# Kernel tuning notes

Measured on AMD Instinct MI355X. Metric: run time of the kernel, lower is better.

The kernel has to match this reference:

```python
import jax, jax.numpy as jnp
import numpy as np

B, C, S, H, W = 1, 256, 64, 32, 128
BLOCKS, HEADS, DH = 2, 8, 32
SCALE = DH ** (-0.5)


def layer_norm(x, w, b, eps=1e-5):
    mu = jnp.mean(x, axis=-1, keepdims=True)
    var = jnp.var(x, axis=-1, keepdims=True)
    return (x - mu) * jax.lax.rsqrt(var + eps) * w + b


def generate_y_for_attn(y, u):
    # y: (B,C,H,W), u: (B,S,S) float -> (B, S^2, 2H, C)
    Bv, Cv, Hv, Wv = y.shape
    Sv = u.shape[1]
    uf = jnp.floor(u).reshape(Bv, Sv * Sv)
    u_left = jnp.clip(uf, 0, Wv - 1).astype(jnp.int32)
    u_right = jnp.clip(uf + 1, 0, Wv - 1).astype(jnp.int32)
    yf = y.reshape(Bv, Cv * Hv, Wv)

    def gather_w(idx):
        idxb = jnp.broadcast_to(idx[:, None, :], (Bv, Cv * Hv, Sv * Sv))
        return jnp.take_along_axis(yf, idxb, axis=2).reshape(Bv, Cv, Hv, Sv * Sv)

    ys = jnp.concatenate([gather_w(u_left), gather_w(u_right)], axis=2)  # (B,C,2H,S2)
    return ys.transpose(0, 3, 2, 1)  # (B, S2, 2H, C)


def cross_attention(x, y, p, i):
    # x: (B,M,C), y: (B,M,N,C)
    q = layer_norm(x, p['ln_q_w'][i], p['ln_q_b'][i]) @ p['Wq'][i]        # (B,M,HD)
    k = layer_norm(y, p['ln_k_w'][i], p['ln_k_b'][i]) @ p['Wk'][i]        # (B,M,N,HD)
    v = layer_norm(y, p['ln_v_w'][i], p['ln_v_b'][i]) @ p['Wv'][i]        # (B,M,N,HD)
    Bv, M, _ = q.shape
    N = k.shape[2]
    q = q.reshape(Bv, M, HEADS, DH)
    k = k.reshape(Bv, M, N, HEADS, DH)
    v = v.reshape(Bv, M, N, HEADS, DH)
    dot = SCALE * jnp.einsum('bmhd,bmnhd->bhmn', q, k)                    # (B,H,M,N)
    attn = jax.nn.softmax(dot, axis=-1)
    a = jnp.einsum('bhmn,bmnhd->bmhd', attn, v).reshape(Bv, M, HEADS * DH)
    z = a @ p['Wproj'][i] + p['bproj'][i]
    z = layer_norm(z, p['ln_pre_w'][i], p['ln_pre_b'][i])
    h = jax.nn.gelu(z @ p['Wm1'][i] + p['bm1'][i], approximate=False)
    z = z + (h @ p['Wm2'][i] + p['bm2'][i])
    return layer_norm(z, p['ln_post_w'][i], p['ln_post_b'][i])


def setup_inputs() -> dict:
    key = jax.random.key(0)
    ks = jax.random.split(key, 16)
    std = 0.02
    inp = {
        'grd2sat': jax.random.normal(ks[0], (B, C, S, S), jnp.float32),
        'grd_x': jax.random.normal(ks[1], (B, C, H, W), jnp.float32),
        'u': jax.random.uniform(ks[2], (B, S, S), jnp.float32) * (W - 1),
        'ln_q_w': jnp.ones((BLOCKS, C)), 'ln_q_b': jnp.zeros((BLOCKS, C)),
        'ln_k_w': jnp.ones((BLOCKS, C)), 'ln_k_b': jnp.zeros((BLOCKS, C)),
        'ln_v_w': jnp.ones((BLOCKS, C)), 'ln_v_b': jnp.zeros((BLOCKS, C)),
        'Wq': std * jax.random.normal(ks[3], (BLOCKS, C, HEADS * DH)),
        'Wk': std * jax.random.normal(ks[4], (BLOCKS, C, HEADS * DH)),
        'Wv': std * jax.random.normal(ks[5], (BLOCKS, C, HEADS * DH)),
        'Wproj': std * jax.random.normal(ks[6], (BLOCKS, HEADS * DH, C)),
        'bproj': jnp.zeros((BLOCKS, C)),
        'ln_pre_w': jnp.ones((BLOCKS, C)), 'ln_pre_b': jnp.zeros((BLOCKS, C)),
        'Wm1': std * jax.random.normal(ks[7], (BLOCKS, C, 2 * C)),
        'bm1': jnp.zeros((BLOCKS, 2 * C)),
        'Wm2': std * jax.random.normal(ks[8], (BLOCKS, 2 * C, C)),
        'bm2': jnp.zeros((BLOCKS, C)),
        'ln_post_w': jnp.ones((BLOCKS, C)), 'ln_post_b': jnp.zeros((BLOCKS, C)),
    }
    return inp


def reference(grd2sat, grd_x, u, ln_q_w, ln_q_b, ln_k_w, ln_k_b, ln_v_w, ln_v_b,
              Wq, Wk, Wv, Wproj, bproj, ln_pre_w, ln_pre_b, Wm1, bm1, Wm2, bm2,
              ln_post_w, ln_post_b):
    p = dict(ln_q_w=ln_q_w, ln_q_b=ln_q_b, ln_k_w=ln_k_w, ln_k_b=ln_k_b,
             ln_v_w=ln_v_w, ln_v_b=ln_v_b, Wq=Wq, Wk=Wk, Wv=Wv, Wproj=Wproj,
             bproj=bproj, ln_pre_w=ln_pre_w, ln_pre_b=ln_pre_b, Wm1=Wm1, bm1=bm1,
             Wm2=Wm2, bm2=bm2, ln_post_w=ln_post_w, ln_post_b=ln_post_b)
    y_attn = generate_y_for_attn(grd_x, u)               # (B, S^2, 2H, C)
    x = grd2sat.reshape(B, C, S * S).transpose(0, 2, 1)  # (B, M, C)
    for i in range(BLOCKS):
        # (Swin self-attention layer omitted; cross-attention stack only.)
        x = cross_attention(x, y_attn, p, i)
    out = x.transpose(0, 2, 1).reshape(B, C, S, S)
    # L2 normalize over channel dim
    norm = jnp.sqrt(jnp.sum(out * out, axis=1, keepdims=True))
    return out / jnp.maximum(norm, 1e-12)
```

## Files before the change

### kernel.cpp

```cpp
#include <hip/hip_runtime.h>
#include <math.h>


#define C_DIM 256
#define M_DIM 4096
#define W_DIM 128
#define H_DIM 32
#define ATT_SCALE 0.17677669529663687f

typedef __attribute__((ext_vector_type(8))) short short8;
typedef __attribute__((ext_vector_type(4))) short short4v;
typedef __attribute__((ext_vector_type(4))) float floatx4;

__device__ __forceinline__ unsigned short f2bf(float f) {
    unsigned u = __float_as_uint(f);
    unsigned r = (u + 0x7fffu + ((u >> 16) & 1u)) >> 16;
    return (unsigned short)r;
}
__device__ __forceinline__ float gelu_exact(float x) {
    return 0.5f * x * (1.0f + erff(x * 0.70710678118654752f));
}

struct PrepArgs {
    const float* grd2sat; float* xcur;
    const float* grd_x;   float* yhat;
    const float* u; int* perm; int4* chunks; int* nchunks;
    const float* win[12]; unsigned short* wout[12]; const float* wlnw[12];
    int wR[12], wC[12], wbase[13];
    const float* fW[10]; const float* flnb[10]; const float* fbase[10];
    float* fout[10];
    int fN[10], fwcol[10], focol[10];
};

__global__ __launch_bounds__(256) void prep_kernel(PrepArgs a) {
    __shared__ float smemf[9024];
    int b = blockIdx.x, t = threadIdx.x;
    if (b < 256) {
        float (*tile)[65] = (float(*)[65])smemf;
        int m0 = (b & 63) << 6, c0 = (b >> 6) << 6;
        for (int it = 0; it < 16; ++it) {
            int idx = it * 256 + t;
            int co = idx >> 6, mo = idx & 63;
            tile[co][mo] = a.grd2sat[(size_t)(c0 + co) * M_DIM + m0 + mo];
        }
        __syncthreads();
        for (int it = 0; it < 16; ++it) {
            int idx = it * 256 + t;
            int mo = idx >> 6, co = idx & 63;
            a.xcur[(size_t)(m0 + mo) * C_DIM + c0 + co] = tile[co][mo];
        }
    } else if (b < 384) {
        int idx = b - 256;
        int h = idx & 31, w0 = (idx >> 5) << 5;
        float (*tile)[33] = (float(*)[33])smemf;
        float (*ps)[32] = (float(*)[32])(smemf + 8448);
        float (*pss)[32] = (float(*)[32])(smemf + 8704);
        float* mu_s = smemf + 8960;
        float* rs_s = smemf + 8992;
        int wo = t & 31, cb = t >> 5;
        for (int it = 0; it < 32; ++it) {
            int c = it * 8 + cb;
            tile[c][wo] = a.grd_x[(size_t)c * (H_DIM * W_DIM) + h * W_DIM + w0 + wo];
        }
        __syncthreads();
        {
            int w = t & 31, part = t >> 5;
            float s = 0.f, ss = 0.f;
            for (int c = part * 32; c < part * 32 + 32; ++c) {
                float x = tile[c][w];
                s += x; ss += x * x;
            }
            ps[part][w] = s; pss[part][w] = ss;
        }
        __syncthreads();
        if (t < 32) {
            float s = 0.f, ss = 0.f;
            for (int p = 0; p < 8; ++p) { s += ps[p][t]; ss += pss[p][t]; }
            float mu = s * (1.f / 256.f);
            float var = ss * (1.f / 256.f) - mu * mu;
            mu_s[t] = mu;
            rs_s[t] = rsqrtf(var + 1e-5f);
        }
        __syncthreads();
        for (int jj = 0; jj < 32; ++jj) {
            float mu = mu_s[jj], rs = rs_s[jj];
            a.yhat[((size_t)(w0 + jj) * H_DIM + h) * C_DIM + t] =
                (tile[t][jj] - mu) * rs;
        }
    } else if (b < 1408) {
        int wI = b - 384;
        int e = 0;
        while (wI >= a.wbase[e + 1]) ++e;
        int tl = wI - a.wbase[e];
        int tilesC = a.wC[e] >> 5;
        int tr = tl / tilesC, tc = tl - tr * tilesC;
        int r0 = tr << 5, c0 = tc << 5;
        const float* in = a.win[e];
        unsigned short* out = a.wout[e];
        const float* lnw = a.wlnw[e];
        int R = a.wR[e], Cc = a.wC[e];
        float (*tile)[33] = (float(*)[33])smemf;
        int rl = t >> 3, cq = (t & 7) << 2;
        float4 v = *(const float4*)&in[(size_t)(r0 + rl) * Cc + c0 + cq];
        if (lnw) {
            float s = lnw[r0 + rl];
            v.x *= s; v.y *= s; v.z *= s; v.w *= s;
        }
        tile[rl][cq + 0] = v.x;
        tile[rl][cq + 1] = v.y;
        tile[rl][cq + 2] = v.z;
        tile[rl][cq + 3] = v.w;
        __syncthreads();
        int cl = t >> 3, rq = (t & 7) << 2;
        ushort4 o;
        o.x = f2bf(tile[rq + 0][cl]);
        o.y = f2bf(tile[rq + 1][cl]);
        o.z = f2bf(tile[rq + 2][cl]);
        o.w = f2bf(tile[rq + 3][cl]);
        *(ushort4*)&out[(size_t)(c0 + cl) * R + r0 + rq] = o;
    } else if (b < 1418) {
        int jj = b - 1408;
        int N = a.fN[jj];
        int wcol = a.fwcol[jj] + t;
        const float* W = a.fW[jj];
        const float* lb = a.flnb[jj];
        float s = a.fbase[jj] ? a.fbase[jj][wcol] : 0.f;
        for (int k = 0; k < 256; ++k) s += lb[k] * W[(size_t)k * N + wcol];
        a.fout[jj][a.focol[jj] + t] = s;
    } else {
        int* hist = (int*)smemf;
        int* cur = (int*)smemf + 128;
        unsigned short* wlb = (unsigned short*)((int*)smemf + 256);
        if (t < 128) hist[t] = 0;
        __syncthreads();
        for (int it = 0; it < 16; ++it) {
            int m = it * 256 + t;
            int wl = (int)floorf(a.u[m]);
            wl = max(0, min(wl, 126));
            wlb[m] = (unsigned short)wl;
            atomicAdd(&hist[wl], 1);
        }
        __syncthreads();
        if (t == 0) {
            int run = 0, nc = 0;
            for (int bkt = 0; bkt < 127; ++bkt) {
                int c = hist[bkt];
                cur[bkt] = run;
                int q0 = run;
                while (c > 0) {
                    int take = min(c, 32);
                    a.chunks[nc] = make_int4(bkt, q0, take, 0);
                    ++nc; q0 += take; c -= take;
                }
                run += hist[bkt];
            }
            *a.nchunks = nc;
        }
        __syncthreads();
        for (int it = 0; it < 16; ++it) {
            int m = it * 256 + t;
            int wl = wlb[m];
            int pos = atomicAdd(&cur[wl], 1);
            a.perm[pos] = m;
        }
    }
}

struct GJ {
    const void* A; const unsigned short* Bt;
    const float* bias; const float* aw; const float* ab;
    const float* rw; const float* rb; const float* res;
    float* wrz; void* out; unsigned short* out2;
    int K, N;
};

template <int LN, int EPI, int OUTM, bool WRZ, bool ABF16>
__device__ __forceinline__ void gemm_core(const GJ& j, short (*As)[264],
                                          short (*Bs)[264], int bm, int by) {
    int t = threadIdx.x;
    int bn = by << 6;
    int wv = t >> 6, lane = t & 63;
    int mt = wv & 1, nt0 = (wv >> 1) << 1;
    int quad = lane >> 4, l16 = lane & 15;
    floatx4 acc0 = {0.f, 0.f, 0.f, 0.f};
    floatx4 acc1 = {0.f, 0.f, 0.f, 0.f};
    const int K = j.K;
    for (int kc = 0; kc < K; kc += 256) {
        if (kc) __syncthreads();
        if (ABF16) {
            int ar = t >> 3, cq = (t & 7) << 5;
            const unsigned short* ap =
                (const unsigned short*)j.A + (size_t)(bm + ar) * K + kc + cq;
#pragma unroll
            for (int c = 0; c < 4; ++c)
                *(uint4*)&As[ar][cq + (c << 3)] = *(const uint4*)(ap + (c << 3));
        } else {
            int ar = t >> 3, cq = (t & 7) << 2;
            const float* ap = (const float*)j.A + (size_t)(bm + ar) * K + kc + cq;
            float4 v[8];
#pragma unroll
            for (int g = 0; g < 8; ++g) v[g] = *(const float4*)(ap + g * 32);
            if (LN >= 1) {
                float s = 0.f, ss = 0.f;
#pragma unroll
                for (int g = 0; g < 8; ++g) {
                    s += v[g].x + v[g].y + v[g].z + v[g].w;
                    ss += v[g].x * v[g].x + v[g].y * v[g].y + v[g].z * v[g].z +
                          v[g].w * v[g].w;
                }
#pragma unroll
                for (int o = 1; o < 8; o <<= 1) {
                    s += __shfl_xor(s, o, 64);
                    ss += __shfl_xor(ss, o, 64);
                }
                float mu = s * (1.f / 256.f);
                float rs = rsqrtf(ss * (1.f / 256.f) - mu * mu + 1e-5f);
#pragma unroll
                for (int g = 0; g < 8; ++g) {
                    v[g].x = (v[g].x - mu) * rs;
                    v[g].y = (v[g].y - mu) * rs;
                    v[g].z = (v[g].z - mu) * rs;
                    v[g].w = (v[g].w - mu) * rs;
                }
                if (LN == 2) {
                    float s2 = 0.f, ss2 = 0.f;
#pragma unroll
                    for (int g = 0; g < 8; ++g) {
                        float4 w4 = *(const float4*)(j.aw + cq + g * 32);
                        float4 b4 = *(const float4*)(j.ab + cq + g * 32);
                        v[g].x = v[g].x * w4.x + b4.x;
                        v[g].y = v[g].y * w4.y + b4.y;
                        v[g].z = v[g].z * w4.z + b4.z;
                        v[g].w = v[g].w * w4.w + b4.w;
                        s2 += v[g].x + v[g].y + v[g].z + v[g].w;
                        ss2 += v[g].x * v[g].x + v[g].y * v[g].y +
                               v[g].z * v[g].z + v[g].w * v[g].w;
                    }
#pragma unroll
                    for (int o = 1; o < 8; o <<= 1) {
                        s2 += __shfl_xor(s2, o, 64);
                        ss2 += __shfl_xor(ss2, o, 64);
                    }
                    float mu2 = s2 * (1.f / 256.f);
                    float rs2 = rsqrtf(ss2 * (1.f / 256.f) - mu2 * mu2 + 1e-5f);
#pragma unroll
                    for (int g = 0; g < 8; ++g) {
                        v[g].x = (v[g].x - mu2) * rs2;
                        v[g].y = (v[g].y - mu2) * rs2;
                        v[g].z = (v[g].z - mu2) * rs2;
                        v[g].w = (v[g].w - mu2) * rs2;
                    }
                }
            }
            if (WRZ) {
                if (by == 0) {
#pragma unroll
                    for (int g = 0; g < 8; ++g)
                        *(float4*)&j.wrz[(size_t)(bm + ar) * 256 + cq + g * 32] =
                            v[g];
                }
            }
#pragma unroll
            for (int g = 0; g < 8; ++g) {
                short4v o;
                o[0] = (short)f2bf(v[g].x);
                o[1] = (short)f2bf(v[g].y);
                o[2] = (short)f2bf(v[g].z);
                o[3] = (short)f2bf(v[g].w);
                *(short4v*)&As[ar][cq + g * 32] = o;
            }
        }
        {
            int br = t >> 2, cq2 = (t & 3) << 3;
            const unsigned short* bp = j.Bt + (size_t)(bn + br) * K + kc + cq2;
#pragma unroll
            for (int g = 0; g < 8; ++g)
                *(short8*)&Bs[br][cq2 + g * 32] = *(const short8*)(bp + g * 32);
        }
        __syncthreads();
#pragma unroll
        for (int k0 = 0; k0 < 8; ++k0) {
            short8 aa = *(const short8*)&As[(mt << 4) + l16][(k0 << 5) + (quad << 3)];
            short8 b0 = *(const short8*)&Bs[(nt0 << 4) + l16][(k0 << 5) + (quad << 3)];
            short8 b1 =
                *(const short8*)&Bs[((nt0 + 1) << 4) + l16][(k0 << 5) + (quad << 3)];
            acc0 = __builtin_amdgcn_mfma_f32_16x16x32_bf16(aa, b0, acc0, 0, 0, 0);
            acc1 = __builtin_amdgcn_mfma_f32_16x16x32_bf16(aa, b1, acc1, 0, 0, 0);
        }
    }
#pragma unroll
    for (int jj = 0; jj < 2; ++jj) {
        const floatx4 accv = jj ? acc1 : acc0;
        int col = bn + ((nt0 + jj) << 4) + l16;
        float bv = j.bias ? j.bias[col] : 0.f;
#pragma unroll
        for (int r = 0; r < 4; ++r) {
            int row = bm + (mt << 4) + (quad << 2) + r;
            float v = accv[r] + bv;
            if (EPI == 1) v = gelu_exact(v);
            if (EPI == 2)
                v += j.res[(size_t)row * 256 + col] * j.rw[col] + j.rb[col];
            if (OUTM == 0) {
                ((float*)j.out)[(size_t)row * j.N + col] = v;
            } else if (OUTM == 1) {
                ((unsigned short*)j.out)[(size_t)row * j.N + col] = f2bf(v);
            } else {
                if (col < 256)
                    ((unsigned short*)j.out)[(size_t)row * 256 + col] = f2bf(v);
                else
                    j.out2[(size_t)(col - 256) * M_DIM + row] = f2bf(v);
            }
        }
    }
}

template <int MODE>
__global__ __launch_bounds__(256) void gemm_mode(GJ j0, GJ j1, GJ j2) {
    __shared__ short As[32][264];
    __shared__ short Bs[64][264];
    int bm = blockIdx.x << 5;
    if (MODE == 0) {
        if ((int)blockIdx.y < 4)
            gemm_core<1, 0, 1, false, false>(j0, As, Bs, bm, blockIdx.y);
        else if ((int)blockIdx.y < 12)
            gemm_core<0, 0, 2, false, false>(j1, As, Bs, bm, blockIdx.y - 4);
        else
            gemm_core<0, 0, 2, false, false>(j2, As, Bs, bm, blockIdx.y - 12);
    } else if (MODE == 1) {
        gemm_core<2, 0, 1, false, false>(j0, As, Bs, bm, blockIdx.y);
    } else if (MODE == 2) {
        gemm_core<0, 0, 0, false, true>(j0, As, Bs, bm, blockIdx.y);
    } else if (MODE == 3) {
        gemm_core<1, 1, 1, true, false>(j0, As, Bs, bm, blockIdx.y);
    } else {
        gemm_core<0, 2, 0, false, true>(j0, As, Bs, bm, blockIdx.y);
    }
}

__global__ __launch_bounds__(256) void attn_kernel(
    const unsigned short* __restrict__ Qb, const unsigned short* __restrict__ Kt,
    const unsigned short* __restrict__ Vt, const int* __restrict__ perm,
    const int4* __restrict__ chunks, const int* __restrict__ nchunks,
    unsigned short* __restrict__ Ao) {
    __shared__ float S[32][69];
    __shared__ short Pb[32][72];
    __shared__ int gperm[32];
    if ((int)blockIdx.x >= *nchunks) return;
    int4 cd = chunks[blockIdx.x];
    int wl = cd.x, qstart = cd.y, qcnt = cd.z;
    int t = threadIdx.x;
    if (t < 32) gperm[t] = (t < qcnt) ? perm[qstart + t] : perm[qstart];
    __syncthreads();
    int wv = t >> 6, lane = t & 63, quad = lane >> 4, l16 = lane & 15;
    int mt = wv & 1, nt0 = (wv >> 1) << 1;
    int ntP = wv >> 1;
    const unsigned short* qp = Qb + (size_t)gperm[(mt << 4) + l16] * 256;
    const unsigned short* kp0 =
        Kt + ((size_t)((wl << 5) + (nt0 << 4) + l16)) * 256;
    const unsigned short* kp1 = kp0 + (16 * 256);
    int sq = t >> 3, sg = t & 7;
    int hb = (int)blockIdx.y << 2;
#pragma unroll 1
    for (int h = hb; h < hb + 4; ++h) {
        {
            short8 aa = *(const short8*)(qp + (h << 5) + (quad << 3));
            short8 b0 = *(const short8*)(kp0 + (h << 5) + (quad << 3));
            short8 b1 = *(const short8*)(kp1 + (h << 5) + (quad << 3));
            floatx4 z = {0.f, 0.f, 0.f, 0.f};
            floatx4 c0 = __builtin_amdgcn_mfma_f32_16x16x32_bf16(aa, b0, z, 0, 0, 0);
            floatx4 c1 = __builtin_amdgcn_mfma_f32_16x16x32_bf16(aa, b1, z, 0, 0, 0);
#pragma unroll
            for (int r = 0; r < 4; ++r) {
                int row = (mt << 4) + (quad << 2) + r;
                S[row][(nt0 << 4) + l16] = c0[r];
                S[row][((nt0 + 1) << 4) + l16] = c1[r];
            }
        }
        __syncthreads();
        {
            float e[8];
            float s = 0.f;
#pragma unroll
            for (int c = 0; c < 8; ++c) {
                e[c] = __expf(S[sq][(sg << 3) + c] * ATT_SCALE);
                s += e[c];
            }
            s += __shfl_xor(s, 1, 64);
            s += __shfl_xor(s, 2, 64);
            s += __shfl_xor(s, 4, 64);
            float ri = 1.f / s;
#pragma unroll
            for (int c = 0; c < 8; ++c)
                Pb[sq][(sg << 3) + c] = (short)f2bf(e[c] * ri);
        }
        __syncthreads();
        {
            const unsigned short* vp =
                Vt + ((size_t)((h << 5) + (ntP << 4) + l16)) * M_DIM + (wl << 5);
            floatx4 acc = {0.f, 0.f, 0.f, 0.f};
#pragma unroll
            for (int ks = 0; ks < 2; ++ks) {
                short8 pa =
                    *(const short8*)&Pb[(mt << 4) + l16][(ks << 5) + (quad << 3)];
                short8 vb = *(const short8*)(vp + (ks << 5) + (quad << 3));
                acc = __builtin_amdgcn_mfma_f32_16x16x32_bf16(pa, vb, acc, 0, 0, 0);
            }
#pragma unroll
            for (int r = 0; r < 4; ++r) {
                int q = (mt << 4) + (quad << 2) + r;
                if (q < qcnt)
                    Ao[(size_t)gperm[q] * 256 + (h << 5) + (ntP << 4) + l16] =
                        f2bf(acc[r]);
            }
        }
    }
}

__global__ __launch_bounds__(256) void out_kernel(const float* __restrict__ X,
                                                  const float* __restrict__ w,
                                                  const float* __restrict__ b,
                                                  float* __restrict__ out) {
    __shared__ float tile[64][65];
    int t = threadIdx.x;
    int mo = t >> 2, q = t & 3;
    int m0 = blockIdx.x << 6;
    const float* p = X + (size_t)(m0 + mo) * C_DIM + (q << 6);
    float4 v[16];
    float s = 0.f, ss = 0.f;
#pragma unroll
    for (int c = 0; c < 16; ++c) {
        v[c] = *(const float4*)(p + c * 4);
        s += v[c].x + v[c].y + v[c].z + v[c].w;
        ss += v[c].x * v[c].x + v[c].y * v[c].y + v[c].z * v[c].z + v[c].w * v[c].w;
    }
    s += __shfl_xor(s, 1, 64); s += __shfl_xor(s, 2, 64);
    ss += __shfl_xor(ss, 1, 64); ss += __shfl_xor(ss, 2, 64);
    float mu = s * (1.f / 256.f);
    float rs = rsqrtf(ss * (1.f / 256.f) - mu * mu + 1e-5f);
    float ss2 = 0.f;
#pragma unroll
    for (int c = 0; c < 16; ++c) {
        float4 w4 = *(const float4*)&w[(q << 6) + c * 4];
        float4 b4 = *(const float4*)&b[(q << 6) + c * 4];
        v[c].x = (v[c].x - mu) * rs * w4.x + b4.x;
        v[c].y = (v[c].y - mu) * rs * w4.y + b4.y;
        v[c].z = (v[c].z - mu) * rs * w4.z + b4.z;
        v[c].w = (v[c].w - mu) * rs * w4.w + b4.w;
        ss2 += v[c].x * v[c].x + v[c].y * v[c].y + v[c].z * v[c].z + v[c].w * v[c].w;
    }
    ss2 += __shfl_xor(ss2, 1, 64); ss2 += __shfl_xor(ss2, 2, 64);
    float sc = 1.f / fmaxf(sqrtf(ss2), 1e-12f);
    for (int cc = 0; cc < 4; ++cc) {
        if (q == cc) {
#pragma unroll
            for (int c = 0; c < 16; ++c) {
                tile[mo][c * 4 + 0] = v[c].x * sc;
                tile[mo][c * 4 + 1] = v[c].y * sc;
                tile[mo][c * 4 + 2] = v[c].z * sc;
                tile[mo][c * 4 + 3] = v[c].w * sc;
            }
        }
        __syncthreads();
        for (int it = 0; it < 16; ++it) {
            int idx = it * 256 + t;
            int co = idx >> 6, mr = idx & 63;
            out[(size_t)((cc << 6) + co) * M_DIM + m0 + mr] = tile[mr][co];
        }
        __syncthreads();
    }
}

extern "C" void kernel_launch(void* const* d_in, const int* in_sizes, int n_in,
                              void* d_out, int out_size, void* d_ws, size_t ws_size,
                              hipStream_t stream) {
    const float* grd2sat = (const float*)d_in[0];
    const float* grd_x   = (const float*)d_in[1];
    const float* u       = (const float*)d_in[2];
    const float* ln_q_w  = (const float*)d_in[3];
    const float* ln_q_b  = (const float*)d_in[4];
    const float* ln_k_w  = (const float*)d_in[5];
    const float* ln_k_b  = (const float*)d_in[6];
    const float* ln_v_w  = (const float*)d_in[7];
    const float* ln_v_b  = (const float*)d_in[8];
    const float* Wq      = (const float*)d_in[9];
    const float* Wk      = (const float*)d_in[10];
    const float* Wv      = (const float*)d_in[11];
    const float* Wproj   = (const float*)d_in[12];
    const float* bproj   = (const float*)d_in[13];
    const float* ln_pre_w = (const float*)d_in[14];
    const float* ln_pre_b = (const float*)d_in[15];
    const float* Wm1     = (const float*)d_in[16];
    const float* bm1     = (const float*)d_in[17];
    const float* Wm2     = (const float*)d_in[18];
    const float* bm2     = (const float*)d_in[19];
    const float* ln_post_w = (const float*)d_in[20];
    const float* ln_post_b = (const float*)d_in[21];

    float* ws   = (float*)d_ws;
    float* yhat = ws;
    float* xcur = ws + 1048576;
    float* zq   = ws + 2097152;
    float* zbuf = ws + 3145728;
    unsigned short* hbuf = (unsigned short*)(ws + 4194304);
    unsigned short* Qb   = (unsigned short*)(ws + 5242880);
    unsigned short* abuf = (unsigned short*)(ws + 5767168);
    unsigned short* Ktab0 = (unsigned short*)(ws + 6291456);
    unsigned short* Vt0   = (unsigned short*)(ws + 6815744);
    unsigned short* Ktab1 = (unsigned short*)(ws + 7340032);
    unsigned short* Vt1   = (unsigned short*)(ws + 7864320);
    unsigned short* Bt    = (unsigned short*)(ws + 8388608);
    float* biasbuf = ws + 8912896;
    int*  perm    = (int*)(ws + 8915456);
    int4* chunks  = (int4*)(ws + 8919552);
    int*  nchunks = (int*)(ws + 8921600);
    const size_t BS = 524288;
    const size_t OQ = 0, OKV = 65536, OP = 196608, OM1 = 262144, OM2 = 393216;

    dim3 b256(256);

    PrepArgs pa;
    pa.grd2sat = grd2sat; pa.xcur = xcur;
    pa.grd_x = grd_x;     pa.yhat = yhat;
    pa.u = u; pa.perm = perm; pa.chunks = chunks; pa.nchunks = nchunks;
    {
        int base = 0;
        for (int i = 0; i < 2; ++i) {
            int e = 6 * i;
            unsigned short* bt = Bt + i * BS;
            pa.win[e+0] = Wq + i * 65536;    pa.wout[e+0] = bt + OQ;
            pa.wlnw[e+0] = ln_q_w + i * 256; pa.wR[e+0] = 256; pa.wC[e+0] = 256;
            pa.win[e+1] = Wk + i * 65536;    pa.wout[e+1] = bt + OKV;
            pa.wlnw[e+1] = ln_k_w + i * 256; pa.wR[e+1] = 256; pa.wC[e+1] = 256;
            pa.win[e+2] = Wv + i * 65536;    pa.wout[e+2] = bt + OKV + 65536;
            pa.wlnw[e+2] = ln_v_w + i * 256; pa.wR[e+2] = 256; pa.wC[e+2] = 256;
            pa.win[e+3] = Wproj + i * 65536; pa.wout[e+3] = bt + OP;
            pa.wlnw[e+3] = nullptr;          pa.wR[e+3] = 256; pa.wC[e+3] = 256;
            pa.win[e+4] = Wm1 + i * 131072;  pa.wout[e+4] = bt + OM1;
            pa.wlnw[e+4] = ln_pre_w + i * 256; pa.wR[e+4] = 256; pa.wC[e+4] = 512;
            pa.win[e+5] = Wm2 + i * 131072;  pa.wout[e+5] = bt + OM2;
            pa.wlnw[e+5] = nullptr;          pa.wR[e+5] = 512; pa.wC[e+5] = 256;
        }
        for (int e = 0; e < 12; ++e) {
            pa.wbase[e] = base;
            base += (pa.wR[e] >> 5) * (pa.wC[e] >> 5);
        }
        pa.wbase[12] = base;
        for (int i = 0; i < 2; ++i) {
            int jb = 5 * i;
            float* bb = biasbuf + i * 1280;
            pa.fW[jb+0] = Wq + i * 65536; pa.flnb[jb+0] = ln_q_b + i * 256;
            pa.fbase[jb+0] = nullptr; pa.fout[jb+0] = bb;
            pa.fN[jb+0] = 256; pa.fwcol[jb+0] = 0; pa.focol[jb+0] = 0;
            pa.fW[jb+1] = Wk + i * 65536; pa.flnb[jb+1] = ln_k_b + i * 256;
            pa.fbase[jb+1] = nullptr; pa.fout[jb+1] = bb + 256;
            pa.fN[jb+1] = 256; pa.fwcol[jb+1] = 0; pa.focol[jb+1] = 0;
            pa.fW[jb+2] = Wv + i * 65536; pa.flnb[jb+2] = ln_v_b + i * 256;
            pa.fbase[jb+2] = nullptr; pa.fout[jb+2] = bb + 256;
            pa.fN[jb+2] = 256; pa.fwcol[jb+2] = 0; pa.focol[jb+2] = 256;
            pa.fW[jb+3] = Wm1 + i * 131072; pa.flnb[jb+3] = ln_pre_b + i * 256;
            pa.fbase[jb+3] = bm1 + i * 512; pa.fout[jb+3] = bb + 768;
            pa.fN[jb+3] = 512; pa.fwcol[jb+3] = 0; pa.focol[jb+3] = 0;
            pa.fW[jb+4] = Wm1 + i * 131072; pa.flnb[jb+4] = ln_pre_b + i * 256;
            pa.fbase[jb+4] = bm1 + i * 512; pa.fout[jb+4] = bb + 768;
            pa.fN[jb+4] = 512; pa.fwcol[jb+4] = 256; pa.focol[jb+4] = 256;
        }
    }
    prep_kernel<<<1419, b256, 0, stream>>>(pa);

    GJ jz = {};
    for (int i = 0; i < 2; ++i) {
        const unsigned short* bt = Bt + i * BS;
        float* bb = biasbuf + i * 1280;
        unsigned short* Kt = i ? Ktab1 : Ktab0;
        unsigned short* Vt = i ? Vt1 : Vt0;

        GJ jq = {};
        jq.A = xcur; jq.Bt = bt + OQ; jq.bias = bb;
        if (i == 1) { jq.aw = ln_post_w; jq.ab = ln_post_b; }
        jq.out = Qb; jq.K = 256; jq.N = 256;
        if (i == 0) {
            GJ jkv0 = {};
            jkv0.A = yhat; jkv0.Bt = Bt + OKV; jkv0.bias = biasbuf + 256;
            jkv0.out = Ktab0; jkv0.out2 = Vt0; jkv0.K = 256; jkv0.N = 512;
            GJ jkv1 = {};
            jkv1.A = yhat; jkv1.Bt = Bt + BS + OKV; jkv1.bias = biasbuf + 1280 + 256;
            jkv1.out = Ktab1; jkv1.out2 = Vt1; jkv1.K = 256; jkv1.N = 512;
            gemm_mode<0><<<dim3(128, 20), b256, 0, stream>>>(jq, jkv0, jkv1);
        } else {
            gemm_mode<1><<<dim3(128, 4), b256, 0, stream>>>(jq, jz, jz);
        }

        attn_kernel<<<dim3(384, 2), b256, 0, stream>>>(Qb, Kt, Vt, perm, chunks,
                                                       nchunks, abuf);

        GJ jp = {};
        jp.A = abuf; jp.Bt = bt + OP; jp.bias = bproj + i * 256;
        jp.out = zq; jp.K = 256; jp.N = 256;
        gemm_mode<2><<<dim3(128, 4), b256, 0, stream>>>(jp, jz, jz);

        GJ jm1 = {};
        jm1.A = zq; jm1.Bt = bt + OM1; jm1.bias = bb + 768;
        jm1.out = hbuf; jm1.wrz = zbuf; jm1.K = 256; jm1.N = 512;
        gemm_mode<3><<<dim3(128, 8), b256, 0, stream>>>(jm1, jz, jz);

        GJ jm2 = {};
        jm2.A = hbuf; jm2.Bt = bt + OM2; jm2.bias = bm2 + i * 256;
        jm2.res = zbuf; jm2.rw = ln_pre_w + i * 256; jm2.rb = ln_pre_b + i * 256;
        jm2.out = xcur; jm2.K = 512; jm2.N = 256;
        gemm_mode<4><<<dim3(128, 4), b256, 0, stream>>>(jm2, jz, jz);
    }
    out_kernel<<<64, b256, 0, stream>>>(xcur, ln_post_w + 256, ln_post_b + 256,
                                        (float*)d_out);
}
```

Measured before the change: 216.4 us.

## Drop LDS staging in GEMM, load MFMA fragments from global; store yhat as bf16

The GEMM core no longer stages A and B tiles through shared memory. Each wave loads its A fragments straight into registers (with LayerNorm applied in registers) and streams B fragments directly from global memory into the MFMAs. This removes the LDS traffic and barriers at the cost of redundant global reads across waves and higher register pressure. The normalized yhat buffer is now stored as bf16, so the K/V GEMMs read half the bytes via the bf16 A path, and the workspace layout is rearranged to match. A small unroll pragma is also added to the bias-folding loop.

```diff
diff --git a/kernel.cpp b/kernel.cpp
--- a/kernel.cpp
+++ b/kernel.cpp
@@ -23,7 +23,7 @@
 
 struct PrepArgs {
     const float* grd2sat; float* xcur;
-    const float* grd_x;   float* yhat;
+    const float* grd_x;   unsigned short* yhat;
     const float* u; int* perm; int4* chunks; int* nchunks;
     const float* win[12]; unsigned short* wout[12]; const float* wlnw[12];
     int wR[12], wC[12], wbase[13];
@@ -85,7 +85,7 @@
         for (int jj = 0; jj < 32; ++jj) {
             float mu = mu_s[jj], rs = rs_s[jj];
             a.yhat[((size_t)(w0 + jj) * H_DIM + h) * C_DIM + t] =
-                (tile[t][jj] - mu) * rs;
+                f2bf((tile[t][jj] - mu) * rs);
         }
     } else if (b < 1408) {
         int wI = b - 384;
@@ -125,6 +125,7 @@
         const float* W = a.fW[jj];
         const float* lb = a.flnb[jj];
         float s = a.fbase[jj] ? a.fbase[jj][wcol] : 0.f;
+#pragma unroll 8
         for (int k = 0; k < 256; ++k) s += lb[k] * W[(size_t)k * N + wcol];
         a.fout[jj][a.focol[jj] + t] = s;
     } else {
@@ -174,119 +175,122 @@
     int K, N;
 };
 
-template <int LN, int EPI, int OUTM, bool WRZ, bool ABF16>
-__device__ __forceinline__ void gemm_core(const GJ& j, short (*As)[264],
-                                          short (*Bs)[264], int bm, int by) {
+template <int LN, int EPI, int OUTM, bool WRZ, bool ABF16, int K32>
+__device__ __forceinline__ void gemm_core(const GJ& j, int bm, int by) {
+    const int K = K32 * 32;
     int t = threadIdx.x;
     int bn = by << 6;
     int wv = t >> 6, lane = t & 63;
     int mt = wv & 1, nt0 = (wv >> 1) << 1;
     int quad = lane >> 4, l16 = lane & 15;
+    int arow = bm + (mt << 4) + l16;
+
+    short8 afr[K32];
+    if (ABF16) {
+        const unsigned short* ap =
+            (const unsigned short*)j.A + (size_t)arow * K + (quad << 3);
+#pragma unroll
+        for (int k0 = 0; k0 < K32; ++k0)
+            afr[k0] = *(const short8*)(ap + (k0 << 5));
+    } else {
+        const float* apf = (const float*)j.A + (size_t)arow * 256 + (quad << 3);
+        float4 v[16];
+#pragma unroll
+        for (int k0 = 0; k0 < 8; ++k0) {
+            v[2 * k0] = *(const float4*)(apf + (k0 << 5));
+            v[2 * k0 + 1] = *(const float4*)(apf + (k0 << 5) + 4);
+        }
+        if (LN >= 1) {
+            float s = 0.f, ss = 0.f;
+#pragma unroll
+            for (int g = 0; g < 16; ++g) {
+                s += v[g].x + v[g].y + v[g].z + v[g].w;
+                ss += v[g].x * v[g].x + v[g].y * v[g].y + v[g].z * v[g].z +
+                      v[g].w * v[g].w;
+            }
+            s += __shfl_xor(s, 16, 64);
+            s += __shfl_xor(s, 32, 64);
+            ss += __shfl_xor(ss, 16, 64);
+            ss += __shfl_xor(ss, 32, 64);
+            float mu = s * (1.f / 256.f);
+            float rs = rsqrtf(ss * (1.f / 256.f) - mu * mu + 1e-5f);
+#pragma unroll
+            for (int g = 0; g < 16; ++g) {
+                v[g].x = (v[g].x - mu) * rs;
+                v[g].y = (v[g].y - mu) * rs;
+                v[g].z = (v[g].z - mu) * rs;
+                v[g].w = (v[g].w - mu) * rs;
+            }
+            if (LN == 2) {
+                float s2 = 0.f, ss2 = 0.f;
+#pragma unroll
+                for (int k0 = 0; k0 < 8; ++k0) {
+                    float4 w0 = *(const float4*)(j.aw + (k0 << 5) + (quad << 3));
+                    float4 w1 = *(const float4*)(j.aw + (k0 << 5) + (quad << 3) + 4);
+                    float4 b0 = *(const float4*)(j.ab + (k0 << 5) + (quad << 3));
+                    float4 b1 = *(const float4*)(j.ab + (k0 << 5) + (quad << 3) + 4);
+                    float4& x0 = v[2 * k0];
+                    float4& x1 = v[2 * k0 + 1];
+                    x0.x = x0.x * w0.x + b0.x; x0.y = x0.y * w0.y + b0.y;
+                    x0.z = x0.z * w0.z + b0.z; x0.w = x0.w * w0.w + b0.w;
+                    x1.x = x1.x * w1.x + b1.x; x1.y = x1.y * w1.y + b1.y;
+                    x1.z = x1.z * w1.z + b1.z; x1.w = x1.w * w1.w + b1.w;
+                    s2 += x0.x + x0.y + x0.z + x0.w + x1.x + x1.y + x1.z + x1.w;
+                    ss2 += x0.x * x0.x + x0.y * x0.y + x0.z * x0.z + x0.w * x0.w +
+                           x1.x * x1.x + x1.y * x1.y + x1.z * x1.z + x1.w * x1.w;
+                }
+                s2 += __shfl_xor(s2, 16, 64);
+                s2 += __shfl_xor(s2, 32, 64);
+                ss2 += __shfl_xor(ss2, 16, 64);
+                ss2 += __shfl_xor(ss2, 32, 64);
+                float mu2 = s2 * (1.f / 256.f);
+                float rs2 = rsqrtf(ss2 * (1.f / 256.f) - mu2 * mu2 + 1e-5f);
+#pragma unroll
+                for (int g = 0; g < 16; ++g) {
+                    v[g].x = (v[g].x - mu2) * rs2;
+                    v[g].y = (v[g].y - mu2) * rs2;
+                    v[g].z = (v[g].z - mu2) * rs2;
+                    v[g].w = (v[g].w - mu2) * rs2;
+                }
+            }
+        }
+        if (WRZ) {
+            if (by == 0 && wv < 2) {
+#pragma unroll
+                for (int k0 = 0; k0 < 8; ++k0) {
+                    *(float4*)&j.wrz[(size_t)arow * 256 + (k0 << 5) + (quad << 3)] =
+                        v[2 * k0];
+                    *(float4*)&j.wrz[(size_t)arow * 256 + (k0 << 5) + (quad << 3) + 4] =
+                        v[2 * k0 + 1];
+                }
+            }
+        }
+#pragma unroll
+        for (int k0 = 0; k0 < 8; ++k0) {
+            short8 f;
+            f[0] = (short)f2bf(v[2 * k0].x);
+            f[1] = (short)f2bf(v[2 * k0].y);
+            f[2] = (short)f2bf(v[2 * k0].z);
+            f[3] = (short)f2bf(v[2 * k0].w);
+            f[4] = (short)f2bf(v[2 * k0 + 1].x);
+            f[5] = (short)f2bf(v[2 * k0 + 1].y);
+            f[6] = (short)f2bf(v[2 * k0 + 1].z);
+            f[7] = (short)f2bf(v[2 * k0 + 1].w);
+            afr[k0] = f;
+        }
+    }
+
     floatx4 acc0 = {0.f, 0.f, 0.f, 0.f};
     floatx4 acc1 = {0.f, 0.f, 0.f, 0.f};
-    const int K = j.K;
-    for (int kc = 0; kc < K; kc += 256) {
-        if (kc) __syncthreads();
-        if (ABF16) {
-            int ar = t >> 3, cq = (t & 7) << 5;
-            const unsigned short* ap =
-                (const unsigned short*)j.A + (size_t)(bm + ar) * K + kc + cq;
-#pragma unroll
-            for (int c = 0; c < 4; ++c)
-                *(uint4*)&As[ar][cq + (c << 3)] = *(const uint4*)(ap + (c << 3));
-        } else {
-            int ar = t >> 3, cq = (t & 7) << 2;
-            const float* ap = (const float*)j.A + (size_t)(bm + ar) * K + kc + cq;
-            float4 v[8];
-#pragma unroll
-            for (int g = 0; g < 8; ++g) v[g] = *(const float4*)(ap + g * 32);
-            if (LN >= 1) {
-                float s = 0.f, ss = 0.f;
-#pragma unroll
-                for (int g = 0; g < 8; ++g) {
-                    s += v[g].x + v[g].y + v[g].z + v[g].w;
-                    ss += v[g].x * v[g].x + v[g].y * v[g].y + v[g].z * v[g].z +
-                          v[g].w * v[g].w;
-                }
-#pragma unroll
-                for (int o = 1; o < 8; o <<= 1) {
-                    s += __shfl_xor(s, o, 64);
-                    ss += __shfl_xor(ss, o, 64);
-                }
-                float mu = s * (1.f / 256.f);
-                float rs = rsqrtf(ss * (1.f / 256.f) - mu * mu + 1e-5f);
-#pragma unroll
-                for (int g = 0; g < 8; ++g) {
-                    v[g].x = (v[g].x - mu) * rs;
-                    v[g].y = (v[g].y - mu) * rs;
-                    v[g].z = (v[g].z - mu) * rs;
-                    v[g].w = (v[g].w - mu) * rs;
-                }
-                if (LN == 2) {
-                    float s2 = 0.f, ss2 = 0.f;
-#pragma unroll
-                    for (int g = 0; g < 8; ++g) {
-                        float4 w4 = *(const float4*)(j.aw + cq + g * 32);
-                        float4 b4 = *(const float4*)(j.ab + cq + g * 32);
-                        v[g].x = v[g].x * w4.x + b4.x;
-                        v[g].y = v[g].y * w4.y + b4.y;
-                        v[g].z = v[g].z * w4.z + b4.z;
-                        v[g].w = v[g].w * w4.w + b4.w;
-                        s2 += v[g].x + v[g].y + v[g].z + v[g].w;
-                        ss2 += v[g].x * v[g].x + v[g].y * v[g].y +
-                               v[g].z * v[g].z + v[g].w * v[g].w;
-                    }
-#pragma unroll
-                    for (int o = 1; o < 8; o <<= 1) {
-                        s2 += __shfl_xor(s2, o, 64);
-                        ss2 += __shfl_xor(ss2, o, 64);
-                    }
-                    float mu2 = s2 * (1.f / 256.f);
-                    float rs2 = rsqrtf(ss2 * (1.f / 256.f) - mu2 * mu2 + 1e-5f);
-#pragma unroll
-                    for (int g = 0; g < 8; ++g) {
-                        v[g].x = (v[g].x - mu2) * rs2;
-                        v[g].y = (v[g].y - mu2) * rs2;
-                        v[g].z = (v[g].z - mu2) * rs2;
-                        v[g].w = (v[g].w - mu2) * rs2;
-                    }
-                }
-            }
-            if (WRZ) {
-                if (by == 0) {
-#pragma unroll
-                    for (int g = 0; g < 8; ++g)
-                        *(float4*)&j.wrz[(size_t)(bm + ar) * 256 + cq + g * 32] =
-                            v[g];
-                }
-            }
-#pragma unroll
-            for (int g = 0; g < 8; ++g) {
-                short4v o;
-                o[0] = (short)f2bf(v[g].x);
-                o[1] = (short)f2bf(v[g].y);
-                o[2] = (short)f2bf(v[g].z);
-                o[3] = (short)f2bf(v[g].w);
-                *(short4v*)&As[ar][cq + g * 32] = o;
-            }
-        }
-        {
-            int br = t >> 2, cq2 = (t & 3) << 3;
-            const unsigned short* bp = j.Bt + (size_t)(bn + br) * K + kc + cq2;
-#pragma unroll
-            for (int g = 0; g < 8; ++g)
-                *(short8*)&Bs[br][cq2 + g * 32] = *(const short8*)(bp + g * 32);
-        }
-        __syncthreads();
-#pragma unroll
-        for (int k0 = 0; k0 < 8; ++k0) {
-            short8 aa = *(const short8*)&As[(mt << 4) + l16][(k0 << 5) + (quad << 3)];
-            short8 b0 = *(const short8*)&Bs[(nt0 << 4) + l16][(k0 << 5) + (quad << 3)];
-            short8 b1 =
-                *(const short8*)&Bs[((nt0 + 1) << 4) + l16][(k0 << 5) + (quad << 3)];
-            acc0 = __builtin_amdgcn_mfma_f32_16x16x32_bf16(aa, b0, acc0, 0, 0, 0);
-            acc1 = __builtin_amdgcn_mfma_f32_16x16x32_bf16(aa, b1, acc1, 0, 0, 0);
-        }
+    const unsigned short* bp0 =
+        j.Bt + (size_t)(bn + (nt0 << 4) + l16) * K + (quad << 3);
+    const unsigned short* bp1 = bp0 + (size_t)16 * K;
+#pragma unroll
+    for (int k0 = 0; k0 < K32; ++k0) {
+        short8 b0 = *(const short8*)(bp0 + (k0 << 5));
+        short8 b1 = *(const short8*)(bp1 + (k0 << 5));
+        acc0 = __builtin_amdgcn_mfma_f32_16x16x32_bf16(afr[k0], b0, acc0, 0, 0, 0);
+        acc1 = __builtin_amdgcn_mfma_f32_16x16x32_bf16(afr[k0], b1, acc1, 0, 0, 0);
     }
 #pragma unroll
     for (int jj = 0; jj < 2; ++jj) {
@@ -296,19 +300,19 @@
 #pragma unroll
         for (int r = 0; r < 4; ++r) {
             int row = bm + (mt << 4) + (quad << 2) + r;
-            float v = accv[r] + bv;
-            if (EPI == 1) v = gelu_exact(v);
+            float val = accv[r] + bv;
+            if (EPI == 1) val = gelu_exact(val);
             if (EPI == 2)
-                v += j.res[(size_t)row * 256 + col] * j.rw[col] + j.rb[col];
+                val += j.res[(size_t)row * 256 + col] * j.rw[col] + j.rb[col];
             if (OUTM == 0) {
-                ((float*)j.out)[(size_t)row * j.N + col] = v;
+                ((float*)j.out)[(size_t)row * j.N + col] = val;
             } else if (OUTM == 1) {
-                ((unsigned short*)j.out)[(size_t)row * j.N + col] = f2bf(v);
+                ((unsigned short*)j.out)[(size_t)row * j.N + col] = f2bf(val);
             } else {
                 if (col < 256)
-                    ((unsigned short*)j.out)[(size_t)row * 256 + col] = f2bf(v);
+                    ((unsigned short*)j.out)[(size_t)row * 256 + col] = f2bf(val);
                 else
-                    j.out2[(size_t)(col - 256) * M_DIM + row] = f2bf(v);
+                    j.out2[(size_t)(col - 256) * M_DIM + row] = f2bf(val);
             }
         }
     }
@@ -316,24 +320,22 @@
 
 template <int MODE>
 __global__ __launch_bounds__(256) void gemm_mode(GJ j0, GJ j1, GJ j2) {
-    __shared__ short As[32][264];
-    __shared__ short Bs[64][264];
     int bm = blockIdx.x << 5;
     if (MODE == 0) {
         if ((int)blockIdx.y < 4)
-            gemm_core<1, 0, 1, false, false>(j0, As, Bs, bm, blockIdx.y);
+            gemm_core<1, 0, 1, false, false, 8>(j0, bm, blockIdx.y);
         else if ((int)blockIdx.y < 12)
-            gemm_core<0, 0, 2, false, false>(j1, As, Bs, bm, blockIdx.y - 4);
+            gemm_core<0, 0, 2, false, true, 8>(j1, bm, blockIdx.y - 4);
         else
-            gemm_core<0, 0, 2, false, false>(j2, As, Bs, bm, blockIdx.y - 12);
+            gemm_core<0, 0, 2, false, true, 8>(j2, bm, blockIdx.y - 12);
     } else if (MODE == 1) {
-        gemm_core<2, 0, 1, false, false>(j0, As, Bs, bm, blockIdx.y);
+        gemm_core<2, 0, 1, false, false, 8>(j0, bm, blockIdx.y);
     } else if (MODE == 2) {
-        gemm_core<0, 0, 0, false, true>(j0, As, Bs, bm, blockIdx.y);
+        gemm_core<0, 0, 0, false, true, 8>(j0, bm, blockIdx.y);
     } else if (MODE == 3) {
-        gemm_core<1, 1, 1, true, false>(j0, As, Bs, bm, blockIdx.y);
+        gemm_core<1, 1, 1, true, false, 8>(j0, bm, blockIdx.y);
     } else {
-        gemm_core<0, 2, 0, false, true>(j0, As, Bs, bm, blockIdx.y);
+        gemm_core<0, 2, 0, false, true, 16>(j0, bm, blockIdx.y);
     }
 }
 
@@ -497,22 +499,23 @@
     const float* ln_post_b = (const float*)d_in[21];
 
     float* ws   = (float*)d_ws;
-    float* yhat = ws;
-    float* xcur = ws + 1048576;
-    float* zq   = ws + 2097152;
-    float* zbuf = ws + 3145728;
-    unsigned short* hbuf = (unsigned short*)(ws + 4194304);
-    unsigned short* Qb   = (unsigned short*)(ws + 5242880);
-    unsigned short* abuf = (unsigned short*)(ws + 5767168);
-    unsigned short* Ktab0 = (unsigned short*)(ws + 6291456);
-    unsigned short* Vt0   = (unsigned short*)(ws + 6815744);
-    unsigned short* Ktab1 = (unsigned short*)(ws + 7340032);
-    unsigned short* Vt1   = (unsigned short*)(ws + 7864320);
-    unsigned short* Bt    = (unsigned short*)(ws + 8388608);
-    float* biasbuf = ws + 8912896;
-    int*  perm    = (int*)(ws + 8915456);
-    int4* chunks  = (int4*)(ws + 8919552);
-    int*  nchunks = (int*)(ws + 8921600);
+    float* xcur = ws;
+    float* zq   = ws + 1048576;
+    float* zbuf = ws + 2097152;
+    unsigned short* U = (unsigned short*)(ws + 3145728);
+    unsigned short* yhat = U;
+    unsigned short* hbuf = U + 1048576;
+    unsigned short* Qb   = U + 3145728;
+    unsigned short* abuf = U + 4194304;
+    unsigned short* Ktab0 = U + 5242880;
+    unsigned short* Vt0   = U + 6291456;
+    unsigned short* Ktab1 = U + 7340032;
+    unsigned short* Vt1   = U + 8388608;
+    unsigned short* Bt    = U + 9437184;
+    float* biasbuf = ws + 8388608;
+    int*  perm    = (int*)(ws + 8391168);
+    int4* chunks  = (int4*)(ws + 8395264);
+    int*  nchunks = (int*)(ws + 8397312);
     const size_t BS = 524288;
     const size_t OQ = 0, OKV = 65536, OP = 196608, OM1 = 262144, OM2 = 393216;
 
```

Measured after the change: 280.7 us. +29.7%, slower.
